# Kernel tuning notes

Measured on AMD Instinct MI355X. Metric: run time of the kernel, lower is better.

The kernel has to match this reference:

```python
import jax, jax.numpy as jnp
import numpy as np

VOCAB = 50257
HIDDEN = 1024
N, T = 32, 2048


def setup_inputs() -> dict:
    key = jax.random.key(0)
    k1, k2, k3 = jax.random.split(key, 3)
    x = jax.random.randint(k1, (N, T), 0, VOCAB)
    # Embedding table (learned params)
    embed = jax.random.normal(k2, (VOCAB, HIDDEN), dtype=jnp.float32) * 0.02
    # Recurrent linear, xavier-normal-ish init
    std = float(np.sqrt(2.0 / (HIDDEN + HIDDEN)))
    W_hh = jax.random.normal(k3, (HIDDEN, HIDDEN), dtype=jnp.float32) * std
    b_h = jnp.zeros((HIDDEN,), dtype=jnp.float32)
    return {"x": x, "embed": embed, "W_hh": W_hh, "b_h": b_h}


def reference(x, embed, W_hh, b_h):
    # h_t = tanh(E[x_t] + h_{t-1} @ W_hh + b_h)
    xh = embed[x]                      # [N, T, H] gather once (same math as per-step gather)
    xh_t = jnp.swapaxes(xh, 0, 1)      # [T, N, H] for scan
    h0 = jnp.zeros((x.shape[0], W_hh.shape[0]), dtype=embed.dtype)

    def step(h, xh_step):
        h_new = jnp.tanh(xh_step + h @ W_hh + b_h)  # [N, H]
        return h_new, h_new

    h_last, z_t = jax.lax.scan(step, h0, xh_t)
    z = jnp.swapaxes(z_t, 0, 1)        # [N, T, H]
    return z, h_last
```

## Files before the change

kernel.cpp:

```cpp
#include <hip/hip_runtime.h>
#include <stdint.h>

#define N_B 32
#define T_S 2048
#define H_D 1024
#define HSLOT ((size_t)N_B * H_D)

template<int CTRL, int ROWMASK>
__device__ __forceinline__ float dpp_add(float x) {
    int t = __builtin_amdgcn_update_dpp(0, __builtin_bit_cast(int, x),
                                        CTRL, ROWMASK, 0xf, true);
    return x + __builtin_bit_cast(float, t);
}

__device__ __forceinline__ unsigned long long wait_pkt(unsigned long long* a,
                                                       unsigned want,
                                                       unsigned long long v) {
    int spins = 0;
    while ((unsigned)(v >> 32) != want) {
        if ((++spins & 63) == 0)
            v = __hip_atomic_fetch_or(a, 0ull, __ATOMIC_RELAXED, __HIP_MEMORY_SCOPE_AGENT);
        else
            v = __hip_atomic_load(a, __ATOMIC_RELAXED, __HIP_MEMORY_SCOPE_AGENT);
    }
    return v;
}

#define PIN_ROW(K) asm volatile("" \
    : "+v"(w[K][0]), "+v"(w[K][1]), "+v"(w[K][2]), "+v"(w[K][3]), \
      "+v"(w[K][4]), "+v"(w[K][5]), "+v"(w[K][6]), "+v"(w[K][7]))

__device__ __forceinline__ float fast_tanh(float x) {
    float xc = fminf(fmaxf(x, -10.0f), 10.0f);
    float e  = __builtin_amdgcn_exp2f(xc * 2.885390081777927f);
    return (e - 1.0f) * __builtin_amdgcn_rcpf(e + 1.0f);
}

__global__ void __attribute__((amdgpu_flat_work_group_size(512, 512),
                               amdgpu_waves_per_eu(2, 2)))
rnn_persist(
    const int* __restrict__ xx, const float* __restrict__ embed,
    const float* __restrict__ W, const float* __restrict__ bh,
    float* __restrict__ out, unsigned long long* __restrict__ hbuf)
{
    __shared__ __align__(8) float h_pair[1024][2];
    __shared__ float xh_lds[2][64];
    __shared__ int   x_lds[2][T_S];

    const int tid = threadIdx.x;
    const int blk = blockIdx.x;
    const int g = ((blk & 7) << 1) | ((blk >> 3) & 1);
    const int s = blk >> 4;
    const int n0 = g * 2;
    const int wv = tid >> 6;
    const int rc = tid & 63;
    const int c_base = s * 64 + wv * 8;

    for (int e = tid; e < 2 * T_S; e += 512) {
        int b = e >> 11, t0 = e & (T_S - 1);
        x_lds[b][t0] = xx[(size_t)(n0 + b) * T_S + t0];
    }
    for (int e = tid; e < 1024; e += 512) {
        h_pair[e][0] = 0.0f; h_pair[e][1] = 0.0f;
    }
    __syncthreads();

    float w[16][8];
#pragma unroll
    for (int k = 0; k < 16; ++k) {
        const float4* p = (const float4*)(W + (size_t)(rc + 64 * k) * H_D + c_base);
        float4 a = p[0]; float4 b4 = p[1];
        w[k][0] = a.x;  w[k][1] = a.y;  w[k][2] = a.z;  w[k][3] = a.w;
        w[k][4] = b4.x; w[k][5] = b4.y; w[k][6] = b4.z; w[k][7] = b4.w;
    }

    const int o  = rc - 48;
    const int ob = (o >> 3) & 1, oj = o & 7;
    int my_n = 0, my_c = 0, xh_idx = 0; float my_bias = 0.0f;
    if (o >= 0) {
        my_c    = c_base + oj;
        my_n    = n0 + ob;
        my_bias = bh[my_c];
        xh_idx  = ob * 64 + (wv * 8 + oj);
    }

    float r_xh = 0.0f;
    if (tid < 128) {
        int b = tid >> 6, c_off = tid & 63;
        r_xh = embed[(size_t)x_lds[b][0] * H_D + (s * 64 + c_off)];
    }

    for (int t = 1; t <= T_S; ++t) {
        if (tid < 128) {
            int b = tid >> 6, c_off = tid & 63;
            xh_lds[b][c_off] = r_xh;
            if (t < T_S)
                r_xh = embed[(size_t)x_lds[b][t] * H_D + (s * 64 + c_off)];
        }
        if (t >= 2) {
            const unsigned tag = (unsigned)(t - 1);
            unsigned long long* base = hbuf + ((size_t)((t - 1) & 1)) * HSLOT;
            unsigned long long* a0 = base + (size_t)n0 * H_D + tid;
            unsigned long long* a1 = a0 + 512;
            unsigned long long* a2 = base + (size_t)(n0 + 1) * H_D + tid;
            unsigned long long* a3 = a2 + 512;
            unsigned long long v0 = __hip_atomic_load(a0, __ATOMIC_RELAXED, __HIP_MEMORY_SCOPE_AGENT);
            unsigned long long v1 = __hip_atomic_load(a1, __ATOMIC_RELAXED, __HIP_MEMORY_SCOPE_AGENT);
            unsigned long long v2 = __hip_atomic_load(a2, __ATOMIC_RELAXED, __HIP_MEMORY_SCOPE_AGENT);
            unsigned long long v3 = __hip_atomic_load(a3, __ATOMIC_RELAXED, __HIP_MEMORY_SCOPE_AGENT);
            v0 = wait_pkt(a0, tag, v0);
            v1 = wait_pkt(a1, tag, v1);
            v2 = wait_pkt(a2, tag, v2);
            v3 = wait_pkt(a3, tag, v3);
            float2 p0 = { __builtin_bit_cast(float, (unsigned)v0),
                          __builtin_bit_cast(float, (unsigned)v2) };
            float2 p1 = { __builtin_bit_cast(float, (unsigned)v1),
                          __builtin_bit_cast(float, (unsigned)v3) };
            ((float2*)h_pair)[tid]       = p0;
            ((float2*)h_pair)[tid + 512] = p1;
        }
        __syncthreads();

        PIN_ROW(0);  PIN_ROW(1);  PIN_ROW(2);  PIN_ROW(3);
        PIN_ROW(4);  PIN_ROW(5);  PIN_ROW(6);  PIN_ROW(7);
        PIN_ROW(8);  PIN_ROW(9);  PIN_ROW(10); PIN_ROW(11);
        PIN_ROW(12); PIN_ROW(13); PIN_ROW(14); PIN_ROW(15);

        float acc0[8], acc1[8];
#pragma unroll
        for (int j = 0; j < 8; ++j) { acc0[j] = 0.0f; acc1[j] = 0.0f; }
        const float2* hp = (const float2*)h_pair;
#pragma unroll
        for (int k = 0; k < 16; ++k) {
            float2 h01 = hp[k * 64 + rc];
#pragma unroll
            for (int j = 0; j < 8; ++j) {
                acc0[j] = fmaf(h01.x, w[k][j], acc0[j]);
                acc1[j] = fmaf(h01.y, w[k][j], acc1[j]);
            }
        }

        float outv = 0.0f;
#pragma unroll
        for (int oo = 0; oo < 16; ++oo) {
            float v = (oo < 8) ? acc0[oo & 7] : acc1[oo & 7];
            v = dpp_add<0xB1,  0xf>(v);
            v = dpp_add<0x4E,  0xf>(v);
            v = dpp_add<0x141, 0xf>(v);
            v = dpp_add<0x140, 0xf>(v);
            v = dpp_add<0x142, 0xa>(v);
            v = dpp_add<0x143, 0xc>(v);
            if (o == oo) outv = v;
        }

        if (o >= 0) {
            float pre = outv + ((const float*)xh_lds)[xh_idx] + my_bias;
            float hv  = fast_tanh(pre);
            unsigned long long p = ((unsigned long long)(unsigned)t << 32)
                                 | (unsigned long long)__builtin_bit_cast(unsigned, hv);
            __hip_atomic_store(hbuf + ((size_t)(t & 1)) * HSLOT + (size_t)my_n * H_D + my_c,
                               p, __ATOMIC_RELAXED, __HIP_MEMORY_SCOPE_AGENT);
            out[((size_t)my_n * T_S + (t - 1)) * H_D + my_c] = hv;
            if (t == T_S)
                out[(size_t)N_B * T_S * H_D + (size_t)my_n * H_D + my_c] = hv;
        }
        __syncthreads();
    }
}

extern "C" void kernel_launch(void* const* d_in, const int* in_sizes, int n_in,
                              void* d_out, int out_size, void* d_ws, size_t ws_size,
                              hipStream_t stream) {
    const int*   xx    = (const int*)d_in[0];
    const float* embed = (const float*)d_in[1];
    const float* W     = (const float*)d_in[2];
    const float* bh    = (const float*)d_in[3];
    float* out = (float*)d_out;
    unsigned long long* hbuf = (unsigned long long*)d_ws;

    hipMemsetAsync(d_ws, 0, 2 * HSLOT * sizeof(unsigned long long), stream);

    void* args[] = { (void*)&xx, (void*)&embed, (void*)&W, (void*)&bh,
                     (void*)&out, (void*)&hbuf };
    hipLaunchCooperativeKernel((const void*)rnn_persist, dim3(256), dim3(512),
                               args, 0, stream);
}
```

Before: 5.830 ms.

## Retile persistent RNN blocks to 4 batch rows by 32 columns

Changes the work split so each block handles four batch rows and a 32-column slice instead of two rows and 64 columns, halving per-thread weight registers and using float4 LDS reads of h. Each block now polls twice as many h packets per step from global memory and depends on twice as many producer blocks, increasing synchronisation fan-in and global traffic.

```diff
diff --git a/kernel.cpp b/kernel.cpp
--- a/kernel.cpp
+++ b/kernel.cpp
@@ -27,8 +27,7 @@
 }
 
 #define PIN_ROW(K) asm volatile("" \
-    : "+v"(w[K][0]), "+v"(w[K][1]), "+v"(w[K][2]), "+v"(w[K][3]), \
-      "+v"(w[K][4]), "+v"(w[K][5]), "+v"(w[K][6]), "+v"(w[K][7]))
+    : "+v"(w[K][0]), "+v"(w[K][1]), "+v"(w[K][2]), "+v"(w[K][3]))
 
 __device__ __forceinline__ float fast_tanh(float x) {
     float xc = fminf(fmaxf(x, -10.0f), 10.0f);
@@ -43,81 +42,90 @@
     const float* __restrict__ W, const float* __restrict__ bh,
     float* __restrict__ out, unsigned long long* __restrict__ hbuf)
 {
-    __shared__ __align__(8) float h_pair[1024][2];
-    __shared__ float xh_lds[2][64];
-    __shared__ int   x_lds[2][T_S];
+    __shared__ __align__(16) float h4[1024][4];
+    __shared__ float xh_lds[4][32];
+    __shared__ int   x_lds[4][T_S];
 
     const int tid = threadIdx.x;
     const int blk = blockIdx.x;
-    const int g = ((blk & 7) << 1) | ((blk >> 3) & 1);
-    const int s = blk >> 4;
-    const int n0 = g * 2;
+    const int g = blk & 7;
+    const int s = blk >> 3;
+    const int n0 = g * 4;
     const int wv = tid >> 6;
     const int rc = tid & 63;
-    const int c_base = s * 64 + wv * 8;
+    const int c_base = s * 32 + wv * 4;
 
-    for (int e = tid; e < 2 * T_S; e += 512) {
+    for (int e = tid; e < 4 * T_S; e += 512) {
         int b = e >> 11, t0 = e & (T_S - 1);
         x_lds[b][t0] = xx[(size_t)(n0 + b) * T_S + t0];
     }
-    for (int e = tid; e < 1024; e += 512) {
-        h_pair[e][0] = 0.0f; h_pair[e][1] = 0.0f;
-    }
+    for (int e = tid; e < 1024; e += 512)
+        ((float4*)h4)[e] = float4{0.0f, 0.0f, 0.0f, 0.0f};
     __syncthreads();
 
-    float w[16][8];
+    float w[16][4];
 #pragma unroll
     for (int k = 0; k < 16; ++k) {
-        const float4* p = (const float4*)(W + (size_t)(rc + 64 * k) * H_D + c_base);
-        float4 a = p[0]; float4 b4 = p[1];
-        w[k][0] = a.x;  w[k][1] = a.y;  w[k][2] = a.z;  w[k][3] = a.w;
-        w[k][4] = b4.x; w[k][5] = b4.y; w[k][6] = b4.z; w[k][7] = b4.w;
+        float4 a = *(const float4*)(W + (size_t)(rc + 64 * k) * H_D + c_base);
+        w[k][0] = a.x; w[k][1] = a.y; w[k][2] = a.z; w[k][3] = a.w;
     }
 
     const int o  = rc - 48;
-    const int ob = (o >> 3) & 1, oj = o & 7;
+    const int ob = (o >> 2) & 3, oj = o & 3;
     int my_n = 0, my_c = 0, xh_idx = 0; float my_bias = 0.0f;
     if (o >= 0) {
         my_c    = c_base + oj;
         my_n    = n0 + ob;
         my_bias = bh[my_c];
-        xh_idx  = ob * 64 + (wv * 8 + oj);
+        xh_idx  = ob * 32 + (wv * 4 + oj);
     }
 
     float r_xh = 0.0f;
     if (tid < 128) {
-        int b = tid >> 6, c_off = tid & 63;
-        r_xh = embed[(size_t)x_lds[b][0] * H_D + (s * 64 + c_off)];
+        int b = tid >> 5, c = tid & 31;
+        r_xh = embed[(size_t)x_lds[b][0] * H_D + (s * 32 + c)];
     }
 
     for (int t = 1; t <= T_S; ++t) {
         if (tid < 128) {
-            int b = tid >> 6, c_off = tid & 63;
-            xh_lds[b][c_off] = r_xh;
+            int b = tid >> 5, c = tid & 31;
+            xh_lds[b][c] = r_xh;
             if (t < T_S)
-                r_xh = embed[(size_t)x_lds[b][t] * H_D + (s * 64 + c_off)];
+                r_xh = embed[(size_t)x_lds[b][t] * H_D + (s * 32 + c)];
         }
         if (t >= 2) {
             const unsigned tag = (unsigned)(t - 1);
             unsigned long long* base = hbuf + ((size_t)((t - 1) & 1)) * HSLOT;
-            unsigned long long* a0 = base + (size_t)n0 * H_D + tid;
-            unsigned long long* a1 = a0 + 512;
-            unsigned long long* a2 = base + (size_t)(n0 + 1) * H_D + tid;
-            unsigned long long* a3 = a2 + 512;
+            unsigned long long* a0 = base + (size_t)(n0 + 0) * H_D + tid;
+            unsigned long long* a1 = base + (size_t)(n0 + 1) * H_D + tid;
+            unsigned long long* a2 = base + (size_t)(n0 + 2) * H_D + tid;
+            unsigned long long* a3 = base + (size_t)(n0 + 3) * H_D + tid;
             unsigned long long v0 = __hip_atomic_load(a0, __ATOMIC_RELAXED, __HIP_MEMORY_SCOPE_AGENT);
             unsigned long long v1 = __hip_atomic_load(a1, __ATOMIC_RELAXED, __HIP_MEMORY_SCOPE_AGENT);
             unsigned long long v2 = __hip_atomic_load(a2, __ATOMIC_RELAXED, __HIP_MEMORY_SCOPE_AGENT);
             unsigned long long v3 = __hip_atomic_load(a3, __ATOMIC_RELAXED, __HIP_MEMORY_SCOPE_AGENT);
+            unsigned long long u0 = __hip_atomic_load(a0 + 512, __ATOMIC_RELAXED, __HIP_MEMORY_SCOPE_AGENT);
+            unsigned long long u1 = __hip_atomic_load(a1 + 512, __ATOMIC_RELAXED, __HIP_MEMORY_SCOPE_AGENT);
+            unsigned long long u2 = __hip_atomic_load(a2 + 512, __ATOMIC_RELAXED, __HIP_MEMORY_SCOPE_AGENT);
+            unsigned long long u3 = __hip_atomic_load(a3 + 512, __ATOMIC_RELAXED, __HIP_MEMORY_SCOPE_AGENT);
             v0 = wait_pkt(a0, tag, v0);
             v1 = wait_pkt(a1, tag, v1);
             v2 = wait_pkt(a2, tag, v2);
             v3 = wait_pkt(a3, tag, v3);
-            float2 p0 = { __builtin_bit_cast(float, (unsigned)v0),
-                          __builtin_bit_cast(float, (unsigned)v2) };
-            float2 p1 = { __builtin_bit_cast(float, (unsigned)v1),
+            u0 = wait_pkt(a0 + 512, tag, u0);
+            u1 = wait_pkt(a1 + 512, tag, u1);
+            u2 = wait_pkt(a2 + 512, tag, u2);
+            u3 = wait_pkt(a3 + 512, tag, u3);
+            float4 p0 = { __builtin_bit_cast(float, (unsigned)v0),
+                          __builtin_bit_cast(float, (unsigned)v1),
+                          __builtin_bit_cast(float, (unsigned)v2),
                           __builtin_bit_cast(float, (unsigned)v3) };
-            ((float2*)h_pair)[tid]       = p0;
-            ((float2*)h_pair)[tid + 512] = p1;
+            float4 p1 = { __builtin_bit_cast(float, (unsigned)u0),
+                          __builtin_bit_cast(float, (unsigned)u1),
+                          __builtin_bit_cast(float, (unsigned)u2),
+                          __builtin_bit_cast(float, (unsigned)u3) };
+            ((float4*)h4)[tid]       = p0;
+            ((float4*)h4)[tid + 512] = p1;
         }
         __syncthreads();
 
@@ -126,24 +134,27 @@
         PIN_ROW(8);  PIN_ROW(9);  PIN_ROW(10); PIN_ROW(11);
         PIN_ROW(12); PIN_ROW(13); PIN_ROW(14); PIN_ROW(15);
 
-        float acc0[8], acc1[8];
+        float acc[4][4];
 #pragma unroll
-        for (int j = 0; j < 8; ++j) { acc0[j] = 0.0f; acc1[j] = 0.0f; }
-        const float2* hp = (const float2*)h_pair;
+        for (int b = 0; b < 4; ++b)
+#pragma unroll
+            for (int j = 0; j < 4; ++j) acc[b][j] = 0.0f;
 #pragma unroll
         for (int k = 0; k < 16; ++k) {
-            float2 h01 = hp[k * 64 + rc];
+            float4 h = ((const float4*)h4)[k * 64 + rc];
 #pragma unroll
-            for (int j = 0; j < 8; ++j) {
-                acc0[j] = fmaf(h01.x, w[k][j], acc0[j]);
-                acc1[j] = fmaf(h01.y, w[k][j], acc1[j]);
+            for (int j = 0; j < 4; ++j) {
+                acc[0][j] = fmaf(h.x, w[k][j], acc[0][j]);
+                acc[1][j] = fmaf(h.y, w[k][j], acc[1][j]);
+                acc[2][j] = fmaf(h.z, w[k][j], acc[2][j]);
+                acc[3][j] = fmaf(h.w, w[k][j], acc[3][j]);
             }
         }
 
         float outv = 0.0f;
 #pragma unroll
         for (int oo = 0; oo < 16; ++oo) {
-            float v = (oo < 8) ? acc0[oo & 7] : acc1[oo & 7];
+            float v = acc[oo >> 2][oo & 3];
             v = dpp_add<0xB1,  0xf>(v);
             v = dpp_add<0x4E,  0xf>(v);
             v = dpp_add<0x141, 0xf>(v);
```

Measured after the change: 9.966 ms. 70.9% more time.
